# Kernel tuning notes

Hardware: AMD Instinct MI355X
Metric: run time of the kernel (lower is better)

Reference implementation:

```python
import jax, jax.numpy as jnp
import numpy as np

NEG_INF = -1e9  # matches masked_fill value -1000000000.0
SLOPE = 0.2     # LeakyReLU negative slope


def setup_inputs() -> dict:
    key = jax.random.key(0)
    k1, k2, k3, k4 = jax.random.split(key, 4)
    B, N, Fin, Fout = 16, 1024, 256, 256
    h = jax.random.normal(k1, (B, N, Fin), dtype=jnp.float32)
    adj = jax.random.randint(k2, (B, N, N), 0, 2, dtype=jnp.int32)
    W = jax.random.normal(k3, (Fin, Fout), dtype=jnp.float32) * (1.0 / np.sqrt(Fin))
    a = jax.random.normal(k4, (2 * Fout,), dtype=jnp.float32) * (1.0 / np.sqrt(2 * Fout))
    return {"h": h, "adj": adj, "W": W, "a": a}


def reference(h, adj, W, a):
    # h: [B,N,Fin], adj: [B,N,N] (0/1), W: [Fin,Fout], a: [2*Fout]
    Fout = W.shape[1]
    Wh = jnp.einsum("bnf,fo->bno", h, W)            # [B,N,Fout]
    a1, a2 = a[:Fout], a[Fout:]
    # e[b,i,j] = leakyrelu( Wh[b,i]·a1 + Wh[b,j]·a2 )  == a(cat(Wh_i, Wh_j))
    f1 = Wh @ a1                                     # [B,N]
    f2 = Wh @ a2                                     # [B,N]
    e = jax.nn.leaky_relu(f1[:, :, None] + f2[:, None, :], negative_slope=SLOPE)
    e = jnp.where(adj == 0, NEG_INF, e)              # mask non-edges
    attention = jax.nn.softmax(e, axis=-1)           # [B,N,N]
    # dropout is identity at eval / p=0
    h_prime = jnp.einsum("bij,bjo->bio", attention, Wh)  # [B,N,Fout]
    return h_prime
```

## Files before the change

kernel.cpp:

```cpp
#include <hip/hip_runtime.h>

typedef __attribute__((ext_vector_type(8))) short bf16x8;
typedef __attribute__((ext_vector_type(4))) float f32x4;

__device__ __forceinline__ unsigned short f2bf(float x) {
    unsigned int u = __float_as_uint(x);
    u += 0x7FFFu + ((u >> 16) & 1u);
    return (unsigned short)(u >> 16);
}

__device__ __forceinline__ void gl_lds16(const void* g, void* l) {
    __builtin_amdgcn_global_load_lds(
        (__attribute__((address_space(1))) void*)((void*)g),
        (__attribute__((address_space(3))) void*)l, 16, 0, 0);
}

__global__ __launch_bounds__(256) void prep(const float* __restrict__ W,
                                            short* __restrict__ WbT) {
    __shared__ float tile[32][33];
    const int t = threadIdx.x;
    const int bx = blockIdx.x & 7, by = blockIdx.x >> 3;
    const int r0 = by * 32, c0 = bx * 32;
    const int lr = t >> 5, lc = t & 31;
#pragma unroll
    for (int q = 0; q < 4; ++q)
        tile[q * 8 + lr][lc] = W[(r0 + q * 8 + lr) * 256 + c0 + lc];
    __syncthreads();
#pragma unroll
    for (int q = 0; q < 4; ++q)
        WbT[(c0 + q * 8 + lr) * 256 + r0 + lc] = (short)f2bf(tile[lc][q * 8 + lr]);
}

__global__ __launch_bounds__(256, 4) void wh_f12(const float* __restrict__ h,
                                                 const short* __restrict__ WbT,
                                                 const float* __restrict__ a,
                                                 short* __restrict__ WhT,
                                                 float* __restrict__ f1,
                                                 float* __restrict__ f2) {
    __shared__ short hA[32][264];
    __shared__ float sp[2][4][32];
    const int t = threadIdx.x;
    const int wid = t >> 6, lane = t & 63;
    const int quad = lane >> 4, l15 = lane & 15;
    const int m0 = blockIdx.x * 32;

#pragma unroll
    for (int rr = 0; rr < 2; ++rr) {
        const int r = rr * 16 + (t >> 4), c0 = (t & 15) * 16;
        const float* hp = h + (size_t)(m0 + r) * 256 + c0;
        float4 v0 = *(const float4*)(hp + 0), v1 = *(const float4*)(hp + 4);
        float4 v2 = *(const float4*)(hp + 8), v3 = *(const float4*)(hp + 12);
        bf16x8 w0, w1;
        w0[0] = (short)f2bf(v0.x); w0[1] = (short)f2bf(v0.y);
        w0[2] = (short)f2bf(v0.z); w0[3] = (short)f2bf(v0.w);
        w0[4] = (short)f2bf(v1.x); w0[5] = (short)f2bf(v1.y);
        w0[6] = (short)f2bf(v1.z); w0[7] = (short)f2bf(v1.w);
        w1[0] = (short)f2bf(v2.x); w1[1] = (short)f2bf(v2.y);
        w1[2] = (short)f2bf(v2.z); w1[3] = (short)f2bf(v2.w);
        w1[4] = (short)f2bf(v3.x); w1[5] = (short)f2bf(v3.y);
        w1[6] = (short)f2bf(v3.z); w1[7] = (short)f2bf(v3.w);
        *(bf16x8*)&hA[r][c0] = w0;
        *(bf16x8*)&hA[r][c0 + 8] = w1;
    }
    __syncthreads();

    f32x4 acc[2][4] = {};
#pragma unroll
    for (int kt = 0; kt < 8; ++kt) {
        const int k0 = kt * 32;
        bf16x8 bv[4];
#pragma unroll
        for (int ft = 0; ft < 4; ++ft)
            bv[ft] = *(const bf16x8*)(WbT + (size_t)(wid * 64 + ft * 16 + l15) * 256 + k0 + quad * 8);
        bf16x8 a0 = *(const bf16x8*)&hA[l15][k0 + quad * 8];
        bf16x8 a1 = *(const bf16x8*)&hA[16 + l15][k0 + quad * 8];
#pragma unroll
        for (int ft = 0; ft < 4; ++ft) {
            acc[0][ft] = __builtin_amdgcn_mfma_f32_16x16x32_bf16(a0, bv[ft], acc[0][ft], 0, 0, 0);
            acc[1][ft] = __builtin_amdgcn_mfma_f32_16x16x32_bf16(a1, bv[ft], acc[1][ft], 0, 0, 0);
        }
    }

    const int b = m0 >> 10;
#pragma unroll
    for (int mf = 0; mf < 2; ++mf) {
        const int il0 = (m0 & 1023) + mf * 16 + quad * 4;
#pragma unroll
        for (int ft = 0; ft < 4; ++ft) {
            const int f = wid * 64 + ft * 16 + l15;
            ushort4 pk;
            pk.x = f2bf(acc[mf][ft][0]);
            pk.y = f2bf(acc[mf][ft][1]);
            pk.z = f2bf(acc[mf][ft][2]);
            pk.w = f2bf(acc[mf][ft][3]);
            *(ushort4*)(WhT + ((size_t)b << 18) + (size_t)f * 1024 + il0) = pk;
        }
    }

    float a1v[4], a2v[4];
#pragma unroll
    for (int ft = 0; ft < 4; ++ft) {
        a1v[ft] = a[wid * 64 + ft * 16 + l15];
        a2v[ft] = a[256 + wid * 64 + ft * 16 + l15];
    }
    float p1[2][4] = {}, p2[2][4] = {};
#pragma unroll
    for (int mf = 0; mf < 2; ++mf)
#pragma unroll
        for (int ft = 0; ft < 4; ++ft)
#pragma unroll
            for (int r = 0; r < 4; ++r) {
                p1[mf][r] += acc[mf][ft][r] * a1v[ft];
                p2[mf][r] += acc[mf][ft][r] * a2v[ft];
            }
#pragma unroll
    for (int off = 1; off < 16; off <<= 1)
#pragma unroll
        for (int mf = 0; mf < 2; ++mf)
#pragma unroll
            for (int r = 0; r < 4; ++r) {
                p1[mf][r] += __shfl_xor(p1[mf][r], off);
                p2[mf][r] += __shfl_xor(p2[mf][r], off);
            }
    if (l15 == 0)
#pragma unroll
        for (int mf = 0; mf < 2; ++mf)
#pragma unroll
            for (int r = 0; r < 4; ++r) {
                sp[0][wid][mf * 16 + quad * 4 + r] = p1[mf][r];
                sp[1][wid][mf * 16 + quad * 4 + r] = p2[mf][r];
            }
    __syncthreads();
    if (t < 32) {
        f1[m0 + t] = sp[0][0][t] + sp[0][1][t] + sp[0][2][t] + sp[0][3][t];
        f2[m0 + t] = sp[1][0][t] + sp[1][1][t] + sp[1][2][t] + sp[1][3][t];
    }
}

__global__ __launch_bounds__(256) void stats_p(const int* __restrict__ adj,
                                               const float* __restrict__ f1g,
                                               const float* __restrict__ f2g,
                                               short* __restrict__ P) {
    const int wid = threadIdx.x >> 6, lane = threadIdx.x & 63;
    const int gid = blockIdx.x * 4 + wid;
    const int b = gid >> 10;
    const int* arow = adj + (size_t)gid * 1024;
    const float* f2b = f2g + (b << 10);
    const float f1r = f1g[gid];

    float e[16];
#pragma unroll
    for (int c = 0; c < 4; ++c) {
        int4 av = *(const int4*)(arow + lane * 4 + c * 256);
        float4 fv = *(const float4*)(f2b + lane * 4 + c * 256);
        float x0 = f1r + fv.x, x1 = f1r + fv.y, x2 = f1r + fv.z, x3 = f1r + fv.w;
        e[c * 4 + 0] = av.x ? fmaxf(x0, 0.2f * x0) : -3.0e38f;
        e[c * 4 + 1] = av.y ? fmaxf(x1, 0.2f * x1) : -3.0e38f;
        e[c * 4 + 2] = av.z ? fmaxf(x2, 0.2f * x2) : -3.0e38f;
        e[c * 4 + 3] = av.w ? fmaxf(x3, 0.2f * x3) : -3.0e38f;
    }
    float m = e[0];
#pragma unroll
    for (int q = 1; q < 16; ++q) m = fmaxf(m, e[q]);
#pragma unroll
    for (int off = 32; off; off >>= 1) m = fmaxf(m, __shfl_xor(m, off));

    float p[16];
    float l = 0.f;
#pragma unroll
    for (int q = 0; q < 16; ++q) { p[q] = __expf(e[q] - m); l += p[q]; }
#pragma unroll
    for (int off = 32; off; off >>= 1) l += __shfl_xor(l, off);
    const float invl = 1.0f / l;

    short* prow = P + (size_t)gid * 1024;
#pragma unroll
    for (int c = 0; c < 4; ++c) {
        ushort4 pk;
        pk.x = f2bf(p[c * 4 + 0] * invl);
        pk.y = f2bf(p[c * 4 + 1] * invl);
        pk.z = f2bf(p[c * 4 + 2] * invl);
        pk.w = f2bf(p[c * 4 + 3] * invl);
        *(ushort4*)(prow + lane * 4 + c * 256) = pk;
    }
}

__global__ __launch_bounds__(256, 2) void agg(const short* __restrict__ P,
                                              const short* __restrict__ WhT,
                                              float* __restrict__ out) {
    __shared__ short As[64 * 128];
    __shared__ short Bs[128 * 128];

    const int t = threadIdx.x;
    const int wid = t >> 6, lane = t & 63;
    const int quad = lane >> 4, l15 = lane & 15;

    const int id = blockIdx.x;
    const int rest = id >> 3;
    const int b = (id & 7) + 8 * (rest & 1);
    const int n0 = ((rest >> 1) & 1) * 128;
    const int m0 = (rest >> 2) * 64;

    const short* Pb = P + ((size_t)b << 20);
    const short* Wb = WhT + ((size_t)b << 18);

    const int rt = t >> 4, sl = t & 15;
    const int wA = ((sl & 8) | ((sl & 7) ^ (rt & 7))) * 8;

    const short* gA[4];
    short* lA[4];
#pragma unroll
    for (int q = 0; q < 4; ++q) {
        gA[q] = Pb + (size_t)(m0 + rt + 16 * q) * 1024 + wA;
        lA[q] = As + t * 8 + q * 2048;
    }
    const short* gB[8];
    short* lB[8];
#pragma unroll
    for (int q = 0; q < 8; ++q) {
        gB[q] = Wb + (size_t)(n0 + rt + 16 * q) * 1024 + wA;
        lB[q] = Bs + t * 8 + q * 2048;
    }

    const int mh = (wid & 1) * 32;
    const int nq = (wid >> 1) * 64;

    f32x4 acc[2][4] = {};

    for (int k0 = 0; k0 < 1024; k0 += 128) {
#pragma unroll
        for (int q = 0; q < 4; ++q) gl_lds16(gA[q] + k0, lA[q]);
#pragma unroll
        for (int q = 0; q < 8; ++q) gl_lds16(gB[q] + k0, lB[q]);
        __syncthreads();

#pragma unroll
        for (int kt = 0; kt < 4; ++kt) {
            const int w = kt * 4 + quad;
            bf16x8 av[2], bv[4];
#pragma unroll
            for (int mf = 0; mf < 2; ++mf) {
                const int r = mh + mf * 16 + l15;
                const int s = (w & 8) | ((w & 7) ^ (r & 7));
                av[mf] = *(const bf16x8*)(As + r * 128 + s * 8);
            }
#pragma unroll
            for (int nf = 0; nf < 4; ++nf) {
                const int r = nq + nf * 16 + l15;
                const int s = (w & 8) | ((w & 7) ^ (r & 7));
                bv[nf] = *(const bf16x8*)(Bs + r * 128 + s * 8);
            }
#pragma unroll
            for (int mf = 0; mf < 2; ++mf)
#pragma unroll
                for (int nf = 0; nf < 4; ++nf)
                    acc[mf][nf] = __builtin_amdgcn_mfma_f32_16x16x32_bf16(av[mf], bv[nf], acc[mf][nf], 0, 0, 0);
        }
        __syncthreads();
    }

#pragma unroll
    for (int mf = 0; mf < 2; ++mf) {
        const int i = m0 + mh + mf * 16 + quad * 4;
#pragma unroll
        for (int nf = 0; nf < 4; ++nf) {
            float* op = out + (size_t)((b << 10) + i) * 256 + n0 + nq + nf * 16 + l15;
            op[0]   = acc[mf][nf][0];
            op[256] = acc[mf][nf][1];
            op[512] = acc[mf][nf][2];
            op[768] = acc[mf][nf][3];
        }
    }
}

extern "C" void kernel_launch(void* const* d_in, const int* in_sizes, int n_in,
                              void* d_out, int out_size, void* d_ws, size_t ws_size,
                              hipStream_t stream) {
    const float* h   = (const float*)d_in[0];
    const int*   adj = (const int*)d_in[1];
    const float* W   = (const float*)d_in[2];
    const float* a   = (const float*)d_in[3];
    float* out = (float*)d_out;

    short* WbT = (short*)d_ws;
    float* f1  = (float*)(WbT + 65536);
    float* f2  = f1 + 16384;
    short* WhT = (short*)(f2 + 16384);
    short* P   = WhT + 16 * 256 * 1024;

    prep<<<64, 256, 0, stream>>>(W, WbT);
    wh_f12<<<512, 256, 0, stream>>>(h, WbT, a, WhT, f1, f2);
    stats_p<<<4096, 256, 0, stream>>>(adj, f1, f2, P);
    agg<<<512, 256, 0, stream>>>(P, WhT, out);
}
```

Before: 152.6 us.

## Recompute softmax probabilities in aggregation from bitmask and per-row stats

The stats kernel no longer writes a dense bf16 probability matrix. It stores a packed adjacency bitmask plus per-row f1, max and inverse sum. The aggregation kernel rebuilds each bf16 probability tile in shared memory from these and f2 (staged in LDS) before the MFMA loop. This removes the write and re-read of a large intermediate, at the cost of recomputing exp in every aggregation block, which is duplicated across column blocks.

```diff
diff --git a/kernel.cpp b/kernel.cpp
--- a/kernel.cpp
+++ b/kernel.cpp
@@ -137,10 +137,11 @@
     }
 }
 
-__global__ __launch_bounds__(256) void stats_p(const int* __restrict__ adj,
-                                               const float* __restrict__ f1g,
-                                               const float* __restrict__ f2g,
-                                               short* __restrict__ P) {
+__global__ __launch_bounds__(256) void stats(const int* __restrict__ adj,
+                                             const float* __restrict__ f1g,
+                                             const float* __restrict__ f2g,
+                                             unsigned char* __restrict__ bm,
+                                             float4* __restrict__ msc) {
     const int wid = threadIdx.x >> 6, lane = threadIdx.x & 63;
     const int gid = blockIdx.x * 4 + wid;
     const int b = gid >> 10;
@@ -149,6 +150,7 @@
     const float f1r = f1g[gid];
 
     float e[16];
+    unsigned int nib[4];
 #pragma unroll
     for (int c = 0; c < 4; ++c) {
         int4 av = *(const int4*)(arow + lane * 4 + c * 256);
@@ -158,6 +160,7 @@
         e[c * 4 + 1] = av.y ? fmaxf(x1, 0.2f * x1) : -3.0e38f;
         e[c * 4 + 2] = av.z ? fmaxf(x2, 0.2f * x2) : -3.0e38f;
         e[c * 4 + 3] = av.w ? fmaxf(x3, 0.2f * x3) : -3.0e38f;
+        nib[c] = (av.x ? 1u : 0u) | (av.y ? 2u : 0u) | (av.z ? 4u : 0u) | (av.w ? 8u : 0u);
     }
     float m = e[0];
 #pragma unroll
@@ -165,31 +168,30 @@
 #pragma unroll
     for (int off = 32; off; off >>= 1) m = fmaxf(m, __shfl_xor(m, off));
 
-    float p[16];
     float l = 0.f;
 #pragma unroll
-    for (int q = 0; q < 16; ++q) { p[q] = __expf(e[q] - m); l += p[q]; }
+    for (int q = 0; q < 16; ++q) l += __expf(e[q] - m);
 #pragma unroll
     for (int off = 32; off; off >>= 1) l += __shfl_xor(l, off);
-    const float invl = 1.0f / l;
-
-    short* prow = P + (size_t)gid * 1024;
+
 #pragma unroll
     for (int c = 0; c < 4; ++c) {
-        ushort4 pk;
-        pk.x = f2bf(p[c * 4 + 0] * invl);
-        pk.y = f2bf(p[c * 4 + 1] * invl);
-        pk.z = f2bf(p[c * 4 + 2] * invl);
-        pk.w = f2bf(p[c * 4 + 3] * invl);
-        *(ushort4*)(prow + lane * 4 + c * 256) = pk;
-    }
-}
-
-__global__ __launch_bounds__(256, 2) void agg(const short* __restrict__ P,
+        unsigned int other = __shfl_xor((int)nib[c], 1);
+        if (!(lane & 1))
+            bm[(size_t)gid * 128 + c * 32 + (lane >> 1)] =
+                (unsigned char)(nib[c] | (other << 4));
+    }
+    if (lane == 0) msc[gid] = make_float4(f1r, m, 1.0f / l, 0.0f);
+}
+
+__global__ __launch_bounds__(256, 2) void agg(const unsigned char* __restrict__ bm,
+                                              const float4* __restrict__ msc,
+                                              const float* __restrict__ f2g,
                                               const short* __restrict__ WhT,
                                               float* __restrict__ out) {
     __shared__ short As[64 * 128];
     __shared__ short Bs[128 * 128];
+    __shared__ float sf2[1024];
 
     const int t = threadIdx.x;
     const int wid = t >> 6, lane = t & 63;
@@ -201,19 +203,12 @@
     const int n0 = ((rest >> 1) & 1) * 128;
     const int m0 = (rest >> 2) * 64;
 
-    const short* Pb = P + ((size_t)b << 20);
     const short* Wb = WhT + ((size_t)b << 18);
 
     const int rt = t >> 4, sl = t & 15;
-    const int wA = ((sl & 8) | ((sl & 7) ^ (rt & 7))) * 8;
-
-    const short* gA[4];
-    short* lA[4];
-#pragma unroll
-    for (int q = 0; q < 4; ++q) {
-        gA[q] = Pb + (size_t)(m0 + rt + 16 * q) * 1024 + wA;
-        lA[q] = As + t * 8 + q * 2048;
-    }
+    const int w = (sl & 8) | ((sl & 7) ^ (rt & 7));
+    const int wA = w * 8;
+
     const short* gB[8];
     short* lB[8];
 #pragma unroll
@@ -222,32 +217,60 @@
         lB[q] = Bs + t * 8 + q * 2048;
     }
 
+    float4 rc[4];
+#pragma unroll
+    for (int q = 0; q < 4; ++q)
+        rc[q] = msc[(b << 10) + m0 + rt + 16 * q];
+    const unsigned char* bmb = bm + (size_t)((b << 10) + m0 + rt) * 128;
+
+    *(float4*)&sf2[t * 4] = *(const float4*)&f2g[(b << 10) + t * 4];
+    __syncthreads();
+
     const int mh = (wid & 1) * 32;
     const int nq = (wid >> 1) * 64;
 
     f32x4 acc[2][4] = {};
 
-    for (int k0 = 0; k0 < 1024; k0 += 128) {
-#pragma unroll
-        for (int q = 0; q < 4; ++q) gl_lds16(gA[q] + k0, lA[q]);
+    for (int it = 0; it < 8; ++it) {
+        const int k0 = it * 128;
 #pragma unroll
         for (int q = 0; q < 8; ++q) gl_lds16(gB[q] + k0, lB[q]);
+
+        unsigned int bits[4];
+#pragma unroll
+        for (int q = 0; q < 4; ++q)
+            bits[q] = bmb[(size_t)q * 16 * 128 + it * 16 + w];
+        float4 fa = *(const float4*)&sf2[k0 + w * 8];
+        float4 fb = *(const float4*)&sf2[k0 + w * 8 + 4];
+        float f2v[8] = {fa.x, fa.y, fa.z, fa.w, fb.x, fb.y, fb.z, fb.w};
+#pragma unroll
+        for (int q = 0; q < 4; ++q) {
+            bf16x8 pv;
+#pragma unroll
+            for (int jj = 0; jj < 8; ++jj) {
+                float x = rc[q].x + f2v[jj];
+                float ee = fmaxf(x, 0.2f * x);
+                float p = __expf(ee - rc[q].y) * rc[q].z;
+                pv[jj] = ((bits[q] >> jj) & 1u) ? (short)f2bf(p) : (short)0;
+            }
+            *(bf16x8*)(As + t * 8 + q * 2048) = pv;
+        }
         __syncthreads();
 
 #pragma unroll
         for (int kt = 0; kt < 4; ++kt) {
-            const int w = kt * 4 + quad;
+            const int wk = kt * 4 + quad;
             bf16x8 av[2], bv[4];
 #pragma unroll
             for (int mf = 0; mf < 2; ++mf) {
                 const int r = mh + mf * 16 + l15;
-                const int s = (w & 8) | ((w & 7) ^ (r & 7));
+                const int s = (wk & 8) | ((wk & 7) ^ (r & 7));
                 av[mf] = *(const bf16x8*)(As + r * 128 + s * 8);
             }
 #pragma unroll
             for (int nf = 0; nf < 4; ++nf) {
                 const int r = nq + nf * 16 + l15;
-                const int s = (w & 8) | ((w & 7) ^ (r & 7));
+                const int s = (wk & 8) | ((wk & 7) ^ (r & 7));
                 bv[nf] = *(const bf16x8*)(Bs + r * 128 + s * 8);
             }
 #pragma unroll
@@ -286,10 +309,11 @@
     float* f1  = (float*)(WbT + 65536);
     float* f2  = f1 + 16384;
     short* WhT = (short*)(f2 + 16384);
-    short* P   = WhT + 16 * 256 * 1024;
+    float4* msc = (float4*)(WhT + 16 * 256 * 1024);
+    unsigned char* bmsk = (unsigned char*)(msc + 16384);
 
     prep<<<64, 256, 0, stream>>>(W, WbT);
     wh_f12<<<512, 256, 0, stream>>>(h, WbT, a, WhT, f1, f2);
-    stats_p<<<4096, 256, 0, stream>>>(adj, f1, f2, P);
-    agg<<<512, 256, 0, stream>>>(P, WhT, out);
-}
+    stats<<<4096, 256, 0, stream>>>(adj, f1, f2, bmsk, msc);
+    agg<<<512, 256, 0, stream>>>(bmsk, msc, f2, WhT, out);
+}
```

Result: slower. 156.1 us (+2.3%).
